# Kernel optimization log

Measured on AMD Instinct MI355X. Metric: run time of the kernel, lower is better.

Reference implementation:

```python
import jax, jax.numpy as jnp
import numpy as np

B, L, K, T, C_IN, C_OUT, TKS = 32, 1855, 7, 40, 8, 32, 5


def setup_inputs() -> dict:
    key = jax.random.key(0)
    k1, k2, k3, k4 = jax.random.split(key, 4)
    x = jax.random.normal(k1, (B, L, T, C_IN), dtype=jnp.float32)
    idx = jax.random.randint(k2, (L, K), 0, L, dtype=jnp.int32)
    missing = jax.random.uniform(k3, (L, K)) < 0.1
    neighbor_indices = jnp.where(missing, jnp.int32(-1), idx)
    fan_in = K * TKS * C_IN
    fan_out = K * TKS * C_OUT
    limit = np.sqrt(6.0 / (fan_in + fan_out))  # glorot uniform
    kernel = jax.random.uniform(k4, (K, TKS, C_IN, C_OUT), dtype=jnp.float32,
                                minval=-limit, maxval=limit)
    bias = jnp.zeros((C_OUT,), dtype=jnp.float32)
    return {"x": x, "neighbor_indices": neighbor_indices, "kernel": kernel, "bias": bias}


def reference(x, neighbor_indices, kernel, bias):
    # x: (B, L, T, C_in); neighbor_indices: (L, K) with -1 = missing
    mask = (neighbor_indices != -1)
    safe_idx = jnp.where(mask, neighbor_indices, 0)
    # gather neighbor features: (B, L, K, T, C_in)
    nf = x[:, safe_idx]
    nf = nf * mask[None, :, :, None, None].astype(x.dtype)
    tks = kernel.shape[1]
    t_out = x.shape[2] - tks + 1
    # valid temporal conv: sum over small fixed tau instead of materializing
    # the (B, L, K, T_out, tks, C_in) framed tensor
    out = jnp.zeros((x.shape[0], x.shape[1], t_out, kernel.shape[-1]), dtype=x.dtype)
    for tau in range(tks):
        out = out + jnp.einsum('blkti,kio->blto',
                               nf[:, :, :, tau:tau + t_out, :], kernel[:, tau])
    return out + bias
```

## Files before the change

### kernel.cpp

```cpp
#include <hip/hip_runtime.h>

constexpr int Bn = 32, Ln = 1855, Kn = 7, Tn = 40, CIn = 8, COn = 32, TKSn = 5, TOn = 36;
constexpr int BG   = 8;
constexpr int KRED = Kn * TKSn * CIn;
constexpr int KPAD = 288;
constexpr int WROW = 296;
constexpr int XS_ELEMS = BG * Kn * Tn * CIn;
constexpr size_t XN = (size_t)Bn * Ln * Tn * CIn;

constexpr size_t WS_WT   = 0;
constexpr size_t WS_ZPAD = 18432;
constexpr size_t WS_XBF  = 18560;
constexpr size_t WS_NEED = WS_XBF + XN * 2;

typedef __attribute__((ext_vector_type(8))) short bf16x8;
typedef __attribute__((ext_vector_type(8))) unsigned short u16x8;
typedef __attribute__((ext_vector_type(4))) float f32x4;

__device__ inline unsigned short f2bf(float f) {
    unsigned u = __builtin_bit_cast(unsigned, f);
    u += 0x7fffu + ((u >> 16) & 1u);
    return (unsigned short)(u >> 16);
}

__device__ inline void gload_lds16(const void* g, void* lds) {
    __builtin_amdgcn_global_load_lds(
        (const __attribute__((address_space(1))) unsigned int*)g,
        (__attribute__((address_space(3))) unsigned int*)lds,
        16, 0, 0);
}


__global__ __launch_bounds__(256) void prep_w(const float* __restrict__ w,
                                              unsigned short* __restrict__ wt,
                                              unsigned short* __restrict__ zpad) {
    const int tid = threadIdx.x;
    for (int p = tid; p < KRED * COn; p += 256) {
        int o  = p & 31;
        int kr = p >> 5;
        wt[o * KPAD + kr] = f2bf(w[p]);
    }
    for (int p = tid; p < COn * (KPAD - KRED); p += 256) {
        int o = p >> 3;
        wt[o * KPAD + KRED + (p & 7)] = 0;
    }
    if (tid < 64) zpad[tid] = 0;
}

__global__ __launch_bounds__(256) void prep_x(const float* __restrict__ x,
                                              unsigned short* __restrict__ xbf) {
    const size_t n8 = XN / 8;
    for (size_t p = (size_t)blockIdx.x * 256 + threadIdx.x; p < n8;
         p += (size_t)gridDim.x * 256) {
        float4 a = ((const float4*)x)[2 * p];
        float4 b = ((const float4*)x)[2 * p + 1];
        u16x8 v;
        v[0] = f2bf(a.x); v[1] = f2bf(a.y); v[2] = f2bf(a.z); v[3] = f2bf(a.w);
        v[4] = f2bf(b.x); v[5] = f2bf(b.y); v[6] = f2bf(b.z); v[7] = f2bf(b.w);
        *(u16x8*)&xbf[p * 8] = v;
    }
}

__global__ __launch_bounds__(256, 4) void conv_mfma2(
    const unsigned short* __restrict__ xbf,
    const int*   __restrict__ nbr,
    const unsigned short* __restrict__ wt,
    const unsigned short* __restrict__ zpad,
    const float* __restrict__ bias,
    float*       __restrict__ out)
{
    __shared__ unsigned short xs[XS_ELEMS + 8];

    const int tid  = threadIdx.x;
    const int l    = blockIdx.x;
    const int bg   = blockIdx.y;
    const int wave = tid >> 6;
    const int lane = tid & 63;

    if (tid < 8) xs[XS_ELEMS + tid] = 0;

    for (int ch = wave; ch < 35; ch += 4) {
        int p   = ch * 64 + lane;
        int row = p / 40;
        int q   = p - row * 40;
        int b_local = row / 7;
        int k       = row - b_local * 7;
        int l2 = nbr[l * Kn + k];
        const unsigned short* src = zpad;
        if (l2 >= 0)
            src = xbf + ((size_t)(bg * BG + b_local) * Ln + l2) * 320 + q * 8;
        gload_lds16(src, &xs[ch * 512]);
    }

    const int quad = lane >> 4;
    const int lrow = lane & 15;
    const int o_base  = (wave & 1) * 16;
    const int rt_base = (wave >> 1) * 9;

    bf16x8 bfrag[9];
    const unsigned short* wrow = wt + (o_base + lrow) * KPAD;
    #pragma unroll
    for (int c = 0; c < 9; ++c)
        bfrag[c] = *(const bf16x8*)(wrow + c * 32 + quad * 8);
    const float bv = bias[o_base + lrow];

    __syncthreads();

    #pragma unroll
    for (int g = 0; g < 3; ++g) {
        const int rt0 = rt_base + g * 3;
        f32x4 acc0 = {0.f,0.f,0.f,0.f}, acc1 = acc0, acc2 = acc0;
        const int m0 = (rt0 + 0) * 16 + lrow;
        const int m1 = (rt0 + 1) * 16 + lrow;
        const int m2 = (rt0 + 2) * 16 + lrow;
        const int bl0 = m0 / 36, t0 = m0 - bl0 * 36;
        const int bl1 = m1 / 36, t1 = m1 - bl1 * 36;
        const int bl2 = m2 / 36, t2 = m2 - bl2 * 36;
        const int base0 = bl0 * 2240 + t0 * 8;
        const int base1 = bl1 * 2240 + t1 * 8;
        const int base2 = bl2 * 2240 + t2 * 8;
        #pragma unroll
        for (int c = 0; c < 9; ++c) {
            const int p = c * 4 + quad;
            const int knbr = p / 5, tau = p - knbr * 5;
            const int koff = knbr * 320 + tau * 8;
            int o0 = base0 + koff, o1 = base1 + koff, o2 = base2 + koff;
            if (c == 8 && quad == 3) { o0 = XS_ELEMS; o1 = XS_ELEMS; o2 = XS_ELEMS; }
            bf16x8 a0 = *(const bf16x8*)&xs[o0];
            bf16x8 a1 = *(const bf16x8*)&xs[o1];
            bf16x8 a2 = *(const bf16x8*)&xs[o2];
            acc0 = __builtin_amdgcn_mfma_f32_16x16x32_bf16(a0, bfrag[c], acc0, 0, 0, 0);
            acc1 = __builtin_amdgcn_mfma_f32_16x16x32_bf16(a1, bfrag[c], acc1, 0, 0, 0);
            acc2 = __builtin_amdgcn_mfma_f32_16x16x32_bf16(a2, bfrag[c], acc2, 0, 0, 0);
        }
        #pragma unroll
        for (int i = 0; i < 3; ++i) {
            const f32x4 acc = (i == 0) ? acc0 : ((i == 1) ? acc1 : acc2);
            const int rt = rt0 + i;
            #pragma unroll
            for (int reg = 0; reg < 4; ++reg) {
                const int m  = rt * 16 + quad * 4 + reg;
                const int bl = m / 36, t = m - bl * 36;
                const size_t off =
                    (((size_t)(bg * BG + bl) * Ln + l) * TOn + t) * COn + o_base + lrow;
                out[off] = acc[reg] + bv;
            }
        }
    }
}

__global__ __launch_bounds__(256) void conv_mfma(
    const float* __restrict__ x, const int* __restrict__ nbr,
    const float* __restrict__ w, const float* __restrict__ bias,
    float* __restrict__ out)
{
    __shared__ unsigned short xs[XS_ELEMS + 8];
    __shared__ unsigned short wt[COn * WROW];

    const int tid = threadIdx.x;
    const int l   = blockIdx.x;
    const int bg  = blockIdx.y;

    for (int p = tid; p < KRED * COn; p += 256) {
        int o  = p & 31;
        int kr = p >> 5;
        wt[o * WROW + kr] = f2bf(w[p]);
    }
    for (int p = tid; p < COn * (WROW - KRED); p += 256) {
        int o = p >> 4;
        wt[o * WROW + KRED + (p & 15)] = 0;
    }
    if (tid < 8) xs[XS_ELEMS + tid] = 0;

    for (int p = tid; p < BG * Kn * 80; p += 256) {
        int b_local = p / 560;
        int r = p - b_local * 560;
        int k = r / 80;
        int q = r - k * 80;
        int l2 = nbr[l * Kn + k];
        float4 v = make_float4(0.f, 0.f, 0.f, 0.f);
        if (l2 >= 0)
            v = ((const float4*)x)[((size_t)(bg * BG + b_local) * Ln + l2) * 80 + q];
        ushort4 pk;
        pk.x = f2bf(v.x); pk.y = f2bf(v.y); pk.z = f2bf(v.z); pk.w = f2bf(v.w);
        *(ushort4*)&xs[p * 4] = pk;
    }
    __syncthreads();

    const int wave = tid >> 6;
    const int lane = tid & 63;
    const int quad = lane >> 4;
    const int lrow = lane & 15;
    const int o_base  = (wave & 1) * 16;
    const int rt_base = (wave >> 1) * 9;

    bf16x8 bfrag[9];
    #pragma unroll
    for (int c = 0; c < 9; ++c)
        bfrag[c] = *(const bf16x8*)&wt[(o_base + lrow) * WROW + c * 32 + quad * 8];

    const float bv = bias[o_base + lrow];

    #pragma unroll
    for (int g = 0; g < 3; ++g) {
        const int rt0 = rt_base + g * 3;
        f32x4 acc0 = {0.f,0.f,0.f,0.f}, acc1 = acc0, acc2 = acc0;
        const int m0 = (rt0 + 0) * 16 + lrow;
        const int m1 = (rt0 + 1) * 16 + lrow;
        const int m2 = (rt0 + 2) * 16 + lrow;
        const int bl0 = m0 / 36, t0 = m0 - bl0 * 36;
        const int bl1 = m1 / 36, t1 = m1 - bl1 * 36;
        const int bl2 = m2 / 36, t2 = m2 - bl2 * 36;
        const int base0 = bl0 * 2240 + t0 * 8;
        const int base1 = bl1 * 2240 + t1 * 8;
        const int base2 = bl2 * 2240 + t2 * 8;
        #pragma unroll
        for (int c = 0; c < 9; ++c) {
            const int p = c * 4 + quad;
            const int knbr = p / 5, tau = p - knbr * 5;
            const int koff = knbr * 320 + tau * 8;
            int o0 = base0 + koff, o1 = base1 + koff, o2 = base2 + koff;
            if (c == 8 && quad == 3) { o0 = XS_ELEMS; o1 = XS_ELEMS; o2 = XS_ELEMS; }
            bf16x8 a0 = *(const bf16x8*)&xs[o0];
            bf16x8 a1 = *(const bf16x8*)&xs[o1];
            bf16x8 a2 = *(const bf16x8*)&xs[o2];
            acc0 = __builtin_amdgcn_mfma_f32_16x16x32_bf16(a0, bfrag[c], acc0, 0, 0, 0);
            acc1 = __builtin_amdgcn_mfma_f32_16x16x32_bf16(a1, bfrag[c], acc1, 0, 0, 0);
            acc2 = __builtin_amdgcn_mfma_f32_16x16x32_bf16(a2, bfrag[c], acc2, 0, 0, 0);
        }
        #pragma unroll
        for (int i = 0; i < 3; ++i) {
            const f32x4 acc = (i == 0) ? acc0 : ((i == 1) ? acc1 : acc2);
            const int rt = rt0 + i;
            #pragma unroll
            for (int reg = 0; reg < 4; ++reg) {
                const int m  = rt * 16 + quad * 4 + reg;
                const int bl = m / 36, t = m - bl * 36;
                const size_t off =
                    (((size_t)(bg * BG + bl) * Ln + l) * TOn + t) * COn + o_base + lrow;
                out[off] = acc[reg] + bv;
            }
        }
    }
}

extern "C" void kernel_launch(void* const* d_in, const int* in_sizes, int n_in,
                              void* d_out, int out_size, void* d_ws, size_t ws_size,
                              hipStream_t stream) {
    const float* x    = (const float*)d_in[0];
    const int*   nbr  = (const int*)d_in[1];
    const float* w    = (const float*)d_in[2];
    const float* bias = (const float*)d_in[3];
    float*       out  = (float*)d_out;

    dim3 grid(Ln, Bn / BG);

    if (ws_size >= WS_NEED && d_ws != nullptr) {
        unsigned short* wt   = (unsigned short*)((char*)d_ws + WS_WT);
        unsigned short* zpad = (unsigned short*)((char*)d_ws + WS_ZPAD);
        unsigned short* xbf  = (unsigned short*)((char*)d_ws + WS_XBF);
        prep_w<<<1, 256, 0, stream>>>(w, wt, zpad);
        prep_x<<<2048, 256, 0, stream>>>(x, xbf);
        conv_mfma2<<<grid, dim3(256), 0, stream>>>(xbf, nbr, wt, zpad, bias, out);
    } else {
        conv_mfma<<<grid, dim3(256), 0, stream>>>(x, nbr, w, bias, out);
    }
}
```

Before: 385.4 us.

## Process four nodes per block with double-buffered LDS gather prefetch

The MFMA conv kernel now handles four consecutive l positions per block, keeping the weight fragments in registers across them. While one node is computed it issues async global-to-LDS loads for the next node into a second buffer. It also raises MFMA priority with s_setprio and lowers the occupancy hint from 4 to 2 blocks per CU. The aim is to hide gather latency and amortise the weight load, at the cost of twice the LDS per block, lower occupancy and a quarter as many blocks.

```diff
diff --git a/kernel.cpp b/kernel.cpp
--- a/kernel.cpp
+++ b/kernel.cpp
@@ -5,7 +5,10 @@
 constexpr int KRED = Kn * TKSn * CIn;
 constexpr int KPAD = 288;
 constexpr int WROW = 296;
-constexpr int XS_ELEMS = BG * Kn * Tn * CIn;
+constexpr int XS_ELEMS  = BG * Kn * Tn * CIn;
+constexpr int XS_STRIDE = XS_ELEMS + 8;
+constexpr int LPB = 4;
+constexpr int NLB = (Ln + LPB - 1) / LPB;
 constexpr size_t XN = (size_t)Bn * Ln * Tn * CIn;
 
 constexpr size_t WS_WT   = 0;
@@ -61,7 +64,7 @@
     }
 }
 
-__global__ __launch_bounds__(256, 4) void conv_mfma2(
+__global__ __launch_bounds__(256, 2) void conv_mfma3(
     const unsigned short* __restrict__ xbf,
     const int*   __restrict__ nbr,
     const unsigned short* __restrict__ wt,
@@ -69,28 +72,43 @@
     const float* __restrict__ bias,
     float*       __restrict__ out)
 {
-    __shared__ unsigned short xs[XS_ELEMS + 8];
+    __shared__ unsigned short xs[2][XS_STRIDE];
 
     const int tid  = threadIdx.x;
-    const int l    = blockIdx.x;
-    const int bg   = blockIdx.y;
     const int wave = tid >> 6;
     const int lane = tid & 63;
-
-    if (tid < 8) xs[XS_ELEMS + tid] = 0;
-
-    for (int ch = wave; ch < 35; ch += 4) {
-        int p   = ch * 64 + lane;
-        int row = p / 40;
-        int q   = p - row * 40;
-        int b_local = row / 7;
-        int k       = row - b_local * 7;
-        int l2 = nbr[l * Kn + k];
-        const unsigned short* src = zpad;
-        if (l2 >= 0)
-            src = xbf + ((size_t)(bg * BG + b_local) * Ln + l2) * 320 + q * 8;
-        gload_lds16(src, &xs[ch * 512]);
-    }
+    const int l0   = blockIdx.x * LPB;
+    const int bg   = blockIdx.y;
+
+    if (tid < 8) { xs[0][XS_ELEMS + tid] = 0; xs[1][XS_ELEMS + tid] = 0; }
+
+    size_t g_off[9]; int g_k[9]; int g_ch[9]; bool g_on[9];
+    #pragma unroll
+    for (int s = 0; s < 9; ++s) {
+        const int ch = wave + 4 * s;
+        g_ch[s] = ch;
+        g_on[s] = (ch < 35);
+        const int chc = g_on[s] ? ch : 0;
+        const int p   = chc * 64 + lane;
+        const int row = p / 40;
+        const int q   = p - row * 40;
+        const int bl  = row / 7;
+        g_k[s]   = row - bl * 7;
+        g_off[s] = (size_t)(bg * BG + bl) * Ln * 320 + (size_t)q * 8;
+    }
+
+    auto stage = [&](int buf, int ll) {
+        const int nb = ll * Kn;
+        #pragma unroll
+        for (int s = 0; s < 9; ++s) {
+            if (g_on[s]) {
+                const int l2 = nbr[nb + g_k[s]];
+                const unsigned short* src = zpad;
+                if (l2 >= 0) src = xbf + g_off[s] + (size_t)l2 * 320;
+                gload_lds16(src, &xs[buf][g_ch[s] * 512]);
+            }
+        }
+    };
 
     const int quad = lane >> 4;
     const int lrow = lane & 15;
@@ -104,7 +122,116 @@
         bfrag[c] = *(const bf16x8*)(wrow + c * 32 + quad * 8);
     const float bv = bias[o_base + lrow];
 
+    auto compute_store = [&](int buf, int l) {
+        const unsigned short* xp = xs[buf];
+        #pragma unroll
+        for (int g = 0; g < 3; ++g) {
+            const int rt0 = rt_base + g * 3;
+            f32x4 acc0 = {0.f,0.f,0.f,0.f}, acc1 = acc0, acc2 = acc0;
+            const int m0 = (rt0 + 0) * 16 + lrow;
+            const int m1 = (rt0 + 1) * 16 + lrow;
+            const int m2 = (rt0 + 2) * 16 + lrow;
+            const int bl0 = m0 / 36, t0 = m0 - bl0 * 36;
+            const int bl1 = m1 / 36, t1 = m1 - bl1 * 36;
+            const int bl2 = m2 / 36, t2 = m2 - bl2 * 36;
+            const int base0 = bl0 * 2240 + t0 * 8;
+            const int base1 = bl1 * 2240 + t1 * 8;
+            const int base2 = bl2 * 2240 + t2 * 8;
+            __builtin_amdgcn_s_setprio(1);
+            #pragma unroll
+            for (int c = 0; c < 9; ++c) {
+                const int p = c * 4 + quad;
+                const int knbr = p / 5, tau = p - knbr * 5;
+                const int koff = knbr * 320 + tau * 8;
+                int o0 = base0 + koff, o1 = base1 + koff, o2 = base2 + koff;
+                if (c == 8 && quad == 3) { o0 = XS_ELEMS; o1 = XS_ELEMS; o2 = XS_ELEMS; }
+                bf16x8 a0 = *(const bf16x8*)&xp[o0];
+                bf16x8 a1 = *(const bf16x8*)&xp[o1];
+                bf16x8 a2 = *(const bf16x8*)&xp[o2];
+                acc0 = __builtin_amdgcn_mfma_f32_16x16x32_bf16(a0, bfrag[c], acc0, 0, 0, 0);
+                acc1 = __builtin_amdgcn_mfma_f32_16x16x32_bf16(a1, bfrag[c], acc1, 0, 0, 0);
+                acc2 = __builtin_amdgcn_mfma_f32_16x16x32_bf16(a2, bfrag[c], acc2, 0, 0, 0);
+            }
+            __builtin_amdgcn_s_setprio(0);
+            #pragma unroll
+            for (int i = 0; i < 3; ++i) {
+                const f32x4 acc = (i == 0) ? acc0 : ((i == 1) ? acc1 : acc2);
+                const int rt = rt0 + i;
+                #pragma unroll
+                for (int reg = 0; reg < 4; ++reg) {
+                    const int m  = rt * 16 + quad * 4 + reg;
+                    const int bl = m / 36, t = m - bl * 36;
+                    const size_t off =
+                        (((size_t)(bg * BG + bl) * Ln + l) * TOn + t) * COn + o_base + lrow;
+                    out[off] = acc[reg] + bv;
+                }
+            }
+        }
+    };
+
+    stage(0, l0);
+    int cur = 0;
+    #pragma unroll
+    for (int j = 0; j < LPB; ++j) {
+        const int l = l0 + j;
+        __syncthreads();
+        if (j + 1 < LPB && l + 1 < Ln) stage(cur ^ 1, l + 1);
+        if (l < Ln) compute_store(cur, l);
+        cur ^= 1;
+    }
+}
+
+__global__ __launch_bounds__(256) void conv_mfma(
+    const float* __restrict__ x, const int* __restrict__ nbr,
+    const float* __restrict__ w, const float* __restrict__ bias,
+    float* __restrict__ out)
+{
+    __shared__ unsigned short xs[XS_ELEMS + 8];
+    __shared__ unsigned short wt[COn * WROW];
+
+    const int tid = threadIdx.x;
+    const int l   = blockIdx.x;
+    const int bg  = blockIdx.y;
+
+    for (int p = tid; p < KRED * COn; p += 256) {
+        int o  = p & 31;
+        int kr = p >> 5;
+        wt[o * WROW + kr] = f2bf(w[p]);
+    }
+    for (int p = tid; p < COn * (WROW - KRED); p += 256) {
+        int o = p >> 4;
+        wt[o * WROW + KRED + (p & 15)] = 0;
+    }
+    if (tid < 8) xs[XS_ELEMS + tid] = 0;
+
+    for (int p = tid; p < BG * Kn * 80; p += 256) {
+        int b_local = p / 560;
+        int r = p - b_local * 560;
+        int k = r / 80;
+        int q = r - k * 80;
+        int l2 = nbr[l * Kn + k];
+        float4 v = make_float4(0.f, 0.f, 0.f, 0.f);
+        if (l2 >= 0)
+            v = ((const float4*)x)[((size_t)(bg * BG + b_local) * Ln + l2) * 80 + q];
+        ushort4 pk;
+        pk.x = f2bf(v.x); pk.y = f2bf(v.y); pk.z = f2bf(v.z); pk.w = f2bf(v.w);
+        *(ushort4*)&xs[p * 4] = pk;
+    }
     __syncthreads();
+
+    const int wave = tid >> 6;
+    const int lane = tid & 63;
+    const int quad = lane >> 4;
+    const int lrow = lane & 15;
+    const int o_base  = (wave & 1) * 16;
+    const int rt_base = (wave >> 1) * 9;
+
+    bf16x8 bfrag[9];
+    #pragma unroll
+    for (int c = 0; c < 9; ++c)
+        bfrag[c] = *(const bf16x8*)&wt[(o_base + lrow) * WROW + c * 32 + quad * 8];
+
+    const float bv = bias[o_base + lrow];
 
     #pragma unroll
     for (int g = 0; g < 3; ++g) {
@@ -149,101 +276,6 @@
     }
 }
 
-__global__ __launch_bounds__(256) void conv_mfma(
-    const float* __restrict__ x, const int* __restrict__ nbr,
-    const float* __restrict__ w, const float* __restrict__ bias,
-    float* __restrict__ out)
-{
-    __shared__ unsigned short xs[XS_ELEMS + 8];
-    __shared__ unsigned short wt[COn * WROW];
-
-    const int tid = threadIdx.x;
-    const int l   = blockIdx.x;
-    const int bg  = blockIdx.y;
-
-    for (int p = tid; p < KRED * COn; p += 256) {
-        int o  = p & 31;
-        int kr = p >> 5;
-        wt[o * WROW + kr] = f2bf(w[p]);
-    }
-    for (int p = tid; p < COn * (WROW - KRED); p += 256) {
-        int o = p >> 4;
-        wt[o * WROW + KRED + (p & 15)] = 0;
-    }
-    if (tid < 8) xs[XS_ELEMS + tid] = 0;
-
-    for (int p = tid; p < BG * Kn * 80; p += 256) {
-        int b_local = p / 560;
-        int r = p - b_local * 560;
-        int k = r / 80;
-        int q = r - k * 80;
-        int l2 = nbr[l * Kn + k];
-        float4 v = make_float4(0.f, 0.f, 0.f, 0.f);
-        if (l2 >= 0)
-            v = ((const float4*)x)[((size_t)(bg * BG + b_local) * Ln + l2) * 80 + q];
-        ushort4 pk;
-        pk.x = f2bf(v.x); pk.y = f2bf(v.y); pk.z = f2bf(v.z); pk.w = f2bf(v.w);
-        *(ushort4*)&xs[p * 4] = pk;
-    }
-    __syncthreads();
-
-    const int wave = tid >> 6;
-    const int lane = tid & 63;
-    const int quad = lane >> 4;
-    const int lrow = lane & 15;
-    const int o_base  = (wave & 1) * 16;
-    const int rt_base = (wave >> 1) * 9;
-
-    bf16x8 bfrag[9];
-    #pragma unroll
-    for (int c = 0; c < 9; ++c)
-        bfrag[c] = *(const bf16x8*)&wt[(o_base + lrow) * WROW + c * 32 + quad * 8];
-
-    const float bv = bias[o_base + lrow];
-
-    #pragma unroll
-    for (int g = 0; g < 3; ++g) {
-        const int rt0 = rt_base + g * 3;
-        f32x4 acc0 = {0.f,0.f,0.f,0.f}, acc1 = acc0, acc2 = acc0;
-        const int m0 = (rt0 + 0) * 16 + lrow;
-        const int m1 = (rt0 + 1) * 16 + lrow;
-        const int m2 = (rt0 + 2) * 16 + lrow;
-        const int bl0 = m0 / 36, t0 = m0 - bl0 * 36;
-        const int bl1 = m1 / 36, t1 = m1 - bl1 * 36;
-        const int bl2 = m2 / 36, t2 = m2 - bl2 * 36;
-        const int base0 = bl0 * 2240 + t0 * 8;
-        const int base1 = bl1 * 2240 + t1 * 8;
-        const int base2 = bl2 * 2240 + t2 * 8;
-        #pragma unroll
-        for (int c = 0; c < 9; ++c) {
-            const int p = c * 4 + quad;
-            const int knbr = p / 5, tau = p - knbr * 5;
-            const int koff = knbr * 320 + tau * 8;
-            int o0 = base0 + koff, o1 = base1 + koff, o2 = base2 + koff;
-            if (c == 8 && quad == 3) { o0 = XS_ELEMS; o1 = XS_ELEMS; o2 = XS_ELEMS; }
-            bf16x8 a0 = *(const bf16x8*)&xs[o0];
-            bf16x8 a1 = *(const bf16x8*)&xs[o1];
-            bf16x8 a2 = *(const bf16x8*)&xs[o2];
-            acc0 = __builtin_amdgcn_mfma_f32_16x16x32_bf16(a0, bfrag[c], acc0, 0, 0, 0);
-            acc1 = __builtin_amdgcn_mfma_f32_16x16x32_bf16(a1, bfrag[c], acc1, 0, 0, 0);
-            acc2 = __builtin_amdgcn_mfma_f32_16x16x32_bf16(a2, bfrag[c], acc2, 0, 0, 0);
-        }
-        #pragma unroll
-        for (int i = 0; i < 3; ++i) {
-            const f32x4 acc = (i == 0) ? acc0 : ((i == 1) ? acc1 : acc2);
-            const int rt = rt0 + i;
-            #pragma unroll
-            for (int reg = 0; reg < 4; ++reg) {
-                const int m  = rt * 16 + quad * 4 + reg;
-                const int bl = m / 36, t = m - bl * 36;
-                const size_t off =
-                    (((size_t)(bg * BG + bl) * Ln + l) * TOn + t) * COn + o_base + lrow;
-                out[off] = acc[reg] + bv;
-            }
-        }
-    }
-}
-
 extern "C" void kernel_launch(void* const* d_in, const int* in_sizes, int n_in,
                               void* d_out, int out_size, void* d_ws, size_t ws_size,
                               hipStream_t stream) {
@@ -253,16 +285,14 @@
     const float* bias = (const float*)d_in[3];
     float*       out  = (float*)d_out;
 
-    dim3 grid(Ln, Bn / BG);
-
     if (ws_size >= WS_NEED && d_ws != nullptr) {
         unsigned short* wt   = (unsigned short*)((char*)d_ws + WS_WT);
         unsigned short* zpad = (unsigned short*)((char*)d_ws + WS_ZPAD);
         unsigned short* xbf  = (unsigned short*)((char*)d_ws + WS_XBF);
         prep_w<<<1, 256, 0, stream>>>(w, wt, zpad);
         prep_x<<<2048, 256, 0, stream>>>(x, xbf);
-        conv_mfma2<<<grid, dim3(256), 0, stream>>>(xbf, nbr, wt, zpad, bias, out);
+        conv_mfma3<<<dim3(NLB, Bn / BG), dim3(256), 0, stream>>>(xbf, nbr, wt, zpad, bias, out);
     } else {
-        conv_mfma<<<grid, dim3(256), 0, stream>>>(x, nbr, w, bias, out);
-    }
-}
+        conv_mfma<<<dim3(Ln, Bn / BG), dim3(256), 0, stream>>>(x, nbr, w, bias, out);
+    }
+}
```

Measured after the change: 405.7 us. 5.3% more time.

## Replace 4-wave conv block with single-wave blocks covering 4 batches and all outputs

Applied to the files above, without the earlier changes.

The main conv kernel now runs one 64-thread wave per block, each handling 4 batches and all 32 output channels. Both weight halves sit in registers, so each A fragment read from LDS feeds two MFMAs, and the block-wide __syncthreads becomes a vmcnt wait. It also broadcasts neighbor indices with a wave shuffle, raises scheduling priority around the MFMA loop, and writes outputs with nontemporal stores. The aim is less LDS traffic per MFMA and more, smaller blocks to raise occupancy. The cost is higher register pressure from 18 weight fragments and 6 accumulators, and twice the block count.

```diff
diff --git a/kernel.cpp b/kernel.cpp
--- a/kernel.cpp
+++ b/kernel.cpp
@@ -6,6 +6,7 @@
 constexpr int KPAD = 288;
 constexpr int WROW = 296;
 constexpr int XS_ELEMS = BG * Kn * Tn * CIn;
+constexpr int XS2 = 4 * Kn * Tn * CIn;
 constexpr size_t XN = (size_t)Bn * Ln * Tn * CIn;
 
 constexpr size_t WS_WT   = 0;
@@ -61,7 +62,7 @@
     }
 }
 
-__global__ __launch_bounds__(256, 4) void conv_mfma2(
+__global__ __launch_bounds__(64, 2) void conv_mfma4(
     const unsigned short* __restrict__ xbf,
     const int*   __restrict__ nbr,
     const unsigned short* __restrict__ wt,
@@ -69,42 +70,151 @@
     const float* __restrict__ bias,
     float*       __restrict__ out)
 {
+    __shared__ unsigned short xs[XS2 + 8];
+
+    const int lane = threadIdx.x;
+    const int l    = blockIdx.x;
+    const int half = blockIdx.y & 1;
+    const int bg   = blockIdx.y >> 1;
+    const int b0   = bg * BG + half * 4;
+
+    if (lane < 8) xs[XS2 + lane] = 0;
+
+    int nv = 0;
+    if (lane < Kn) nv = nbr[l * Kn + lane];
+
+    #pragma unroll
+    for (int s = 0; s < 18; ++s) {
+        if (s < 17 || lane < 32) {
+            const int u   = s * 64 + lane;
+            const int row = u / 40;
+            const int q   = u - row * 40;
+            const int bl  = row / 7;
+            const int k   = row - bl * 7;
+            const int l2  = __shfl(nv, k);
+            const unsigned short* src = zpad;
+            if (l2 >= 0)
+                src = xbf + ((size_t)(b0 + bl) * Ln + l2) * 320 + q * 8;
+            gload_lds16(src, &xs[s * 512]);
+        }
+    }
+
+    const int quad = lane >> 4;
+    const int lrow = lane & 15;
+
+    bf16x8 bfrag[2][9];
+    #pragma unroll
+    for (int oh = 0; oh < 2; ++oh)
+        #pragma unroll
+        for (int c = 0; c < 9; ++c)
+            bfrag[oh][c] = *(const bf16x8*)(wt + (oh * 16 + lrow) * KPAD + c * 32 + quad * 8);
+    const float bv0 = bias[lrow];
+    const float bv1 = bias[16 + lrow];
+
+    asm volatile("s_waitcnt vmcnt(0)" ::: "memory");
+
+    #pragma unroll
+    for (int g = 0; g < 3; ++g) {
+        const int rt0 = g * 3;
+        f32x4 a00 = {0.f,0.f,0.f,0.f};
+        f32x4 acc00 = a00, acc01 = a00, acc10 = a00, acc11 = a00, acc20 = a00, acc21 = a00;
+        const int m0 = (rt0 + 0) * 16 + lrow;
+        const int m1 = (rt0 + 1) * 16 + lrow;
+        const int m2 = (rt0 + 2) * 16 + lrow;
+        const int bl0 = m0 / 36, t0 = m0 - bl0 * 36;
+        const int bl1 = m1 / 36, t1 = m1 - bl1 * 36;
+        const int bl2 = m2 / 36, t2 = m2 - bl2 * 36;
+        const int base0 = bl0 * 2240 + t0 * 8;
+        const int base1 = bl1 * 2240 + t1 * 8;
+        const int base2 = bl2 * 2240 + t2 * 8;
+        __builtin_amdgcn_s_setprio(1);
+        #pragma unroll
+        for (int c = 0; c < 9; ++c) {
+            const int p = c * 4 + quad;
+            const int knbr = p / 5, tau = p - knbr * 5;
+            const int koff = knbr * 320 + tau * 8;
+            int o0 = base0 + koff, o1 = base1 + koff, o2 = base2 + koff;
+            if (c == 8 && quad == 3) { o0 = XS2; o1 = XS2; o2 = XS2; }
+            bf16x8 a0 = *(const bf16x8*)&xs[o0];
+            bf16x8 a1 = *(const bf16x8*)&xs[o1];
+            bf16x8 a2 = *(const bf16x8*)&xs[o2];
+            acc00 = __builtin_amdgcn_mfma_f32_16x16x32_bf16(a0, bfrag[0][c], acc00, 0, 0, 0);
+            acc01 = __builtin_amdgcn_mfma_f32_16x16x32_bf16(a0, bfrag[1][c], acc01, 0, 0, 0);
+            acc10 = __builtin_amdgcn_mfma_f32_16x16x32_bf16(a1, bfrag[0][c], acc10, 0, 0, 0);
+            acc11 = __builtin_amdgcn_mfma_f32_16x16x32_bf16(a1, bfrag[1][c], acc11, 0, 0, 0);
+            acc20 = __builtin_amdgcn_mfma_f32_16x16x32_bf16(a2, bfrag[0][c], acc20, 0, 0, 0);
+            acc21 = __builtin_amdgcn_mfma_f32_16x16x32_bf16(a2, bfrag[1][c], acc21, 0, 0, 0);
+        }
+        __builtin_amdgcn_s_setprio(0);
+        #pragma unroll
+        for (int i = 0; i < 3; ++i) {
+            const f32x4 c0 = (i == 0) ? acc00 : ((i == 1) ? acc10 : acc20);
+            const f32x4 c1 = (i == 0) ? acc01 : ((i == 1) ? acc11 : acc21);
+            const int rt = rt0 + i;
+            #pragma unroll
+            for (int reg = 0; reg < 4; ++reg) {
+                const int m  = rt * 16 + quad * 4 + reg;
+                const int bl = m / 36, t = m - bl * 36;
+                const size_t off =
+                    (((size_t)(b0 + bl) * Ln + l) * TOn + t) * COn + lrow;
+                __builtin_nontemporal_store(c0[reg] + bv0, &out[off]);
+                __builtin_nontemporal_store(c1[reg] + bv1, &out[off + 16]);
+            }
+        }
+    }
+}
+
+__global__ __launch_bounds__(256) void conv_mfma(
+    const float* __restrict__ x, const int* __restrict__ nbr,
+    const float* __restrict__ w, const float* __restrict__ bias,
+    float* __restrict__ out)
+{
     __shared__ unsigned short xs[XS_ELEMS + 8];
-
-    const int tid  = threadIdx.x;
-    const int l    = blockIdx.x;
-    const int bg   = blockIdx.y;
+    __shared__ unsigned short wt[COn * WROW];
+
+    const int tid = threadIdx.x;
+    const int l   = blockIdx.x;
+    const int bg  = blockIdx.y;
+
+    for (int p = tid; p < KRED * COn; p += 256) {
+        int o  = p & 31;
+        int kr = p >> 5;
+        wt[o * WROW + kr] = f2bf(w[p]);
+    }
+    for (int p = tid; p < COn * (WROW - KRED); p += 256) {
+        int o = p >> 4;
+        wt[o * WROW + KRED + (p & 15)] = 0;
+    }
+    if (tid < 8) xs[XS_ELEMS + tid] = 0;
+
+    for (int p = tid; p < BG * Kn * 80; p += 256) {
+        int b_local = p / 560;
+        int r = p - b_local * 560;
+        int k = r / 80;
+        int q = r - k * 80;
+        int l2 = nbr[l * Kn + k];
+        float4 v = make_float4(0.f, 0.f, 0.f, 0.f);
+        if (l2 >= 0)
+            v = ((const float4*)x)[((size_t)(bg * BG + b_local) * Ln + l2) * 80 + q];
+        ushort4 pk;
+        pk.x = f2bf(v.x); pk.y = f2bf(v.y); pk.z = f2bf(v.z); pk.w = f2bf(v.w);
+        *(ushort4*)&xs[p * 4] = pk;
+    }
+    __syncthreads();
+
     const int wave = tid >> 6;
     const int lane = tid & 63;
-
-    if (tid < 8) xs[XS_ELEMS + tid] = 0;
-
-    for (int ch = wave; ch < 35; ch += 4) {
-        int p   = ch * 64 + lane;
-        int row = p / 40;
-        int q   = p - row * 40;
-        int b_local = row / 7;
-        int k       = row - b_local * 7;
-        int l2 = nbr[l * Kn + k];
-        const unsigned short* src = zpad;
-        if (l2 >= 0)
-            src = xbf + ((size_t)(bg * BG + b_local) * Ln + l2) * 320 + q * 8;
-        gload_lds16(src, &xs[ch * 512]);
-    }
-
     const int quad = lane >> 4;
     const int lrow = lane & 15;
     const int o_base  = (wave & 1) * 16;
     const int rt_base = (wave >> 1) * 9;
 
     bf16x8 bfrag[9];
-    const unsigned short* wrow = wt + (o_base + lrow) * KPAD;
     #pragma unroll
     for (int c = 0; c < 9; ++c)
-        bfrag[c] = *(const bf16x8*)(wrow + c * 32 + quad * 8);
+        bfrag[c] = *(const bf16x8*)&wt[(o_base + lrow) * WROW + c * 32 + quad * 8];
+
     const float bv = bias[o_base + lrow];
-
-    __syncthreads();
 
     #pragma unroll
     for (int g = 0; g < 3; ++g) {
@@ -149,101 +259,6 @@
     }
 }
 
-__global__ __launch_bounds__(256) void conv_mfma(
-    const float* __restrict__ x, const int* __restrict__ nbr,
-    const float* __restrict__ w, const float* __restrict__ bias,
-    float* __restrict__ out)
-{
-    __shared__ unsigned short xs[XS_ELEMS + 8];
-    __shared__ unsigned short wt[COn * WROW];
-
-    const int tid = threadIdx.x;
-    const int l   = blockIdx.x;
-    const int bg  = blockIdx.y;
-
-    for (int p = tid; p < KRED * COn; p += 256) {
-        int o  = p & 31;
-        int kr = p >> 5;
-        wt[o * WROW + kr] = f2bf(w[p]);
-    }
-    for (int p = tid; p < COn * (WROW - KRED); p += 256) {
-        int o = p >> 4;
-        wt[o * WROW + KRED + (p & 15)] = 0;
-    }
-    if (tid < 8) xs[XS_ELEMS + tid] = 0;
-
-    for (int p = tid; p < BG * Kn * 80; p += 256) {
-        int b_local = p / 560;
-        int r = p - b_local * 560;
-        int k = r / 80;
-        int q = r - k * 80;
-        int l2 = nbr[l * Kn + k];
-        float4 v = make_float4(0.f, 0.f, 0.f, 0.f);
-        if (l2 >= 0)
-            v = ((const float4*)x)[((size_t)(bg * BG + b_local) * Ln + l2) * 80 + q];
-        ushort4 pk;
-        pk.x = f2bf(v.x); pk.y = f2bf(v.y); pk.z = f2bf(v.z); pk.w = f2bf(v.w);
-        *(ushort4*)&xs[p * 4] = pk;
-    }
-    __syncthreads();
-
-    const int wave = tid >> 6;
-    const int lane = tid & 63;
-    const int quad = lane >> 4;
-    const int lrow = lane & 15;
-    const int o_base  = (wave & 1) * 16;
-    const int rt_base = (wave >> 1) * 9;
-
-    bf16x8 bfrag[9];
-    #pragma unroll
-    for (int c = 0; c < 9; ++c)
-        bfrag[c] = *(const bf16x8*)&wt[(o_base + lrow) * WROW + c * 32 + quad * 8];
-
-    const float bv = bias[o_base + lrow];
-
-    #pragma unroll
-    for (int g = 0; g < 3; ++g) {
-        const int rt0 = rt_base + g * 3;
-        f32x4 acc0 = {0.f,0.f,0.f,0.f}, acc1 = acc0, acc2 = acc0;
-        const int m0 = (rt0 + 0) * 16 + lrow;
-        const int m1 = (rt0 + 1) * 16 + lrow;
-        const int m2 = (rt0 + 2) * 16 + lrow;
-        const int bl0 = m0 / 36, t0 = m0 - bl0 * 36;
-        const int bl1 = m1 / 36, t1 = m1 - bl1 * 36;
-        const int bl2 = m2 / 36, t2 = m2 - bl2 * 36;
-        const int base0 = bl0 * 2240 + t0 * 8;
-        const int base1 = bl1 * 2240 + t1 * 8;
-        const int base2 = bl2 * 2240 + t2 * 8;
-        #pragma unroll
-        for (int c = 0; c < 9; ++c) {
-            const int p = c * 4 + quad;
-            const int knbr = p / 5, tau = p - knbr * 5;
-            const int koff = knbr * 320 + tau * 8;
-            int o0 = base0 + koff, o1 = base1 + koff, o2 = base2 + koff;
-            if (c == 8 && quad == 3) { o0 = XS_ELEMS; o1 = XS_ELEMS; o2 = XS_ELEMS; }
-            bf16x8 a0 = *(const bf16x8*)&xs[o0];
-            bf16x8 a1 = *(const bf16x8*)&xs[o1];
-            bf16x8 a2 = *(const bf16x8*)&xs[o2];
-            acc0 = __builtin_amdgcn_mfma_f32_16x16x32_bf16(a0, bfrag[c], acc0, 0, 0, 0);
-            acc1 = __builtin_amdgcn_mfma_f32_16x16x32_bf16(a1, bfrag[c], acc1, 0, 0, 0);
-            acc2 = __builtin_amdgcn_mfma_f32_16x16x32_bf16(a2, bfrag[c], acc2, 0, 0, 0);
-        }
-        #pragma unroll
-        for (int i = 0; i < 3; ++i) {
-            const f32x4 acc = (i == 0) ? acc0 : ((i == 1) ? acc1 : acc2);
-            const int rt = rt0 + i;
-            #pragma unroll
-            for (int reg = 0; reg < 4; ++reg) {
-                const int m  = rt * 16 + quad * 4 + reg;
-                const int bl = m / 36, t = m - bl * 36;
-                const size_t off =
-                    (((size_t)(bg * BG + bl) * Ln + l) * TOn + t) * COn + o_base + lrow;
-                out[off] = acc[reg] + bv;
-            }
-        }
-    }
-}
-
 extern "C" void kernel_launch(void* const* d_in, const int* in_sizes, int n_in,
                               void* d_out, int out_size, void* d_ws, size_t ws_size,
                               hipStream_t stream) {
@@ -253,16 +268,14 @@
     const float* bias = (const float*)d_in[3];
     float*       out  = (float*)d_out;
 
-    dim3 grid(Ln, Bn / BG);
-
     if (ws_size >= WS_NEED && d_ws != nullptr) {
         unsigned short* wt   = (unsigned short*)((char*)d_ws + WS_WT);
         unsigned short* zpad = (unsigned short*)((char*)d_ws + WS_ZPAD);
         unsigned short* xbf  = (unsigned short*)((char*)d_ws + WS_XBF);
         prep_w<<<1, 256, 0, stream>>>(w, wt, zpad);
         prep_x<<<2048, 256, 0, stream>>>(x, xbf);
-        conv_mfma2<<<grid, dim3(256), 0, stream>>>(xbf, nbr, wt, zpad, bias, out);
+        conv_mfma4<<<dim3(Ln, 8), dim3(64), 0, stream>>>(xbf, nbr, wt, zpad, bias, out);
     } else {
-        conv_mfma<<<grid, dim3(256), 0, stream>>>(x, nbr, w, bias, out);
-    }
-}
+        conv_mfma<<<dim3(Ln, Bn / BG), dim3(256), 0, stream>>>(x, nbr, w, bias, out);
+    }
+}
```

New measurement: 369.6 us. 4.1% less time.
